# Optimization experiments

Measured on AMD Instinct MI355X. Metric: run time of the kernel, lower is better.

The kernel has to match this reference:

```python
import jax, jax.numpy as jnp
import numpy as np

DIM = 1024
H = 16
DH = DIM // H
NF = 64
EPS = 1e-6


def setup_inputs() -> dict:
    key = jax.random.key(0)
    ks = jax.random.split(key, 10)
    B, L = 4, 4096
    s = 1.0 / np.sqrt(DIM)
    x = jax.random.normal(ks[0], (B, L, DIM), dtype=jnp.float32)
    Wq = jax.random.normal(ks[1], (DIM, DIM), dtype=jnp.float32) * s
    Wk = jax.random.normal(ks[2], (DIM, DIM), dtype=jnp.float32) * s
    Wv = jax.random.normal(ks[3], (DIM, DIM), dtype=jnp.float32) * s
    Wo = jax.random.normal(ks[4], (DIM, DIM), dtype=jnp.float32) * s
    bq = jax.random.normal(ks[5], (DIM,), dtype=jnp.float32) * s
    bk = jax.random.normal(ks[6], (DIM,), dtype=jnp.float32) * s
    bv = jax.random.normal(ks[7], (DIM,), dtype=jnp.float32) * s
    bo = jax.random.normal(ks[8], (DIM,), dtype=jnp.float32) * s
    # random-feature buffer: [num_repeats=1, H, DH, NF]; use repeat 0
    Wrf = jax.random.normal(ks[9], (1, H, DH, NF), dtype=jnp.float32)
    return {"x": x, "Wq": Wq, "bq": bq, "Wk": Wk, "bk": bk, "Wv": Wv,
            "bv": bv, "Wo": Wo, "bo": bo, "Wrf": Wrf}


def reference(x, Wq, bq, Wk, bk, Wv, bv, Wo, bo, Wrf):
    B, L, _ = x.shape
    W0 = Wrf[0]  # [H, DH, NF]

    def split_heads(y):
        return y.reshape(B, L, H, DH).transpose(0, 2, 1, 3)  # [B,H,L,DH]

    q = split_heads(x @ Wq.T + bq)
    k = split_heads(x @ Wk.T + bk)
    v = split_heads(x @ Wv.T + bv)

    # key summary: logits [B,H,L,NF], softmax over flattened (L*NF)
    logits = jnp.einsum('bhld,hdf->bhlf', k, W0) \
             - 0.5 * jnp.sum(k * k, axis=-1, keepdims=True)
    alpha = jax.nn.softmax(logits.reshape(B, H, L * NF), axis=2)
    alpha = alpha.reshape(B, H, L, NF)
    N = jnp.einsum('bhlf,bhld->bhfd', alpha, v)  # [B,H,NF,DH]
    D = jnp.sum(alpha, axis=2)                   # [B,H,NF]

    # query feature map: per-position softmax over features
    phi = jax.nn.softmax(jnp.einsum('bhld,hdf->bhlf', q, W0), axis=-1)

    num = jnp.einsum('bhlf,bhfd->bhld', phi, N)
    den = jnp.einsum('bhlf,bhf->bhl', phi, D)
    out = num / (den[..., None] + EPS)

    ctx = out.transpose(0, 2, 1, 3).reshape(B, L, DIM)
    return ctx @ Wo.T + bo
```

## Files before the change

### kernel.cpp

```cpp
#include <hip/hip_runtime.h>
#include <hip/hip_bf16.h>

constexpr int NB   = 4;
constexpr int SL   = 4096;
constexpr int DIMC = 1024;
constexpr int NH   = 16;
constexpr int DHC  = 64;
constexpr int NFC  = 64;
constexpr int NCHK = 8;
constexpr float FEPS = 1e-6f;

typedef __attribute__((ext_vector_type(8))) short bf16x8_t;
typedef __attribute__((ext_vector_type(4))) float f32x4_t;
typedef __attribute__((ext_vector_type(4))) short s16x4_t;

__device__ __forceinline__ void load_lds_16B(const short* g, short* l) {
  __builtin_amdgcn_global_load_lds(
      (__attribute__((address_space(1))) void*)(g),
      (__attribute__((address_space(3))) void*)(l), 16, 0, 0);
}

__global__ __launch_bounds__(256) void cast_f32_to_bf16(
    const float* __restrict__ in, short* __restrict__ out, int n)
{
  const int i = (blockIdx.x * 256 + threadIdx.x) * 4;
  if (i >= n) return;
  const f32x4_t v = *(const f32x4_t*)(in + i);
  s16x4_t o;
#pragma unroll
  for (int j = 0; j < 4; j++) {
    __hip_bfloat16 h = __float2bfloat16(v[j]);
    o[j] = *(short*)&h;
  }
  *(s16x4_t*)(out + i) = o;
}

__global__ __launch_bounds__(256) void prep_w0t_kernel(
    const float* __restrict__ Wrf, short* __restrict__ Whi, short* __restrict__ Wlo)
{
  const int h = blockIdx.x;
  for (int t = threadIdx.x; t < 4096; t += 256) {
    const int f = t >> 6, dh = t & 63;
    const float w = Wrf[(size_t)h * 4096 + dh * 64 + f];
    __hip_bfloat16 hi = __float2bfloat16(w);
    const float rem = w - __bfloat162float(hi);
    __hip_bfloat16 lo = __float2bfloat16(rem);
    Whi[(size_t)h * 4096 + t] = *(short*)&hi;
    Wlo[(size_t)h * 4096 + t] = *(short*)&lo;
  }
}

__global__ __launch_bounds__(256) void fuse_w0_kernel(
    const float* __restrict__ Wq, const float* __restrict__ bq,
    const float* __restrict__ Wrf,
    short* __restrict__ Wfh, short* __restrict__ Wfl, float* __restrict__ bqf)
{
  const int h = blockIdx.x, cb = blockIdx.y;
  __shared__ float sWq[64][64];
  __shared__ float sW0[64][64];
  for (int idx = threadIdx.x; idx < 4096; idx += 256) {
    const int d = idx >> 6, e = idx & 63;
    sWq[d][e] = Wq[(size_t)(h * 64 + d) * 1024 + cb * 64 + e];
    sW0[d][e] = Wrf[(size_t)h * 4096 + d * 64 + e];
  }
  __syncthreads();
  for (int idx = threadIdx.x; idx < 4096; idx += 256) {
    const int f = idx >> 6, cc = idx & 63;
    float acc = 0.f;
#pragma unroll
    for (int d = 0; d < 64; d++) acc = fmaf(sWq[d][cc], sW0[d][f], acc);
    const __hip_bfloat16 hi = __float2bfloat16(acc);
    const float rem = acc - __bfloat162float(hi);
    const __hip_bfloat16 lo = __float2bfloat16(rem);
    Wfh[(size_t)(h * 64 + f) * 1024 + cb * 64 + cc] = *(const short*)&hi;
    Wfl[(size_t)(h * 64 + f) * 1024 + cb * 64 + cc] = *(const short*)&lo;
  }
  if (cb == 0 && threadIdx.x < 64) {
    const int f = threadIdx.x;
    float acc = 0.f;
#pragma unroll
    for (int d = 0; d < 64; d++) acc = fmaf(bq[h * 64 + d], sW0[d][f], acc);
    bqf[h * 64 + f] = acc;
  }
}

template <int MODE>
__global__ __launch_bounds__(256) void gemm_lds_kernel(
    const short* __restrict__ A, const short* __restrict__ W,
    const float* __restrict__ bias, void* __restrict__ C0,
    void* __restrict__ C1, float* __restrict__ Ks)
{
  constexpr int K = 1024, N = 1024;
  const int lane = threadIdx.x & 63;
  const int wid  = threadIdx.x >> 6;
  const int sub  = lane & 15;
  const int quad = lane >> 4;
  const int wr   = (wid >> 1) * 64;
  const int wc   = (wid & 1) * 64;
  const int row0 = blockIdx.x * 128;
  const int col0 = blockIdx.y * 128;

  __shared__ short As[128 * 64];
  __shared__ short Bs[128 * 64];

  f32x4_t acc[4][4] = {};

  const int srow = lane >> 3;
  for (int k0 = 0; k0 < K; k0 += 64) {
#pragma unroll
    for (int t = 0; t < 4; t++) {
      const int R   = wid * 32 + t * 8;
      const int row = R + srow;
      const int c   = (lane & 7) ^ (row & 7);
      load_lds_16B(A + (size_t)(row0 + row) * K + k0 + c * 8, As + R * 64);
      load_lds_16B(W + (size_t)(col0 + row) * K + k0 + c * 8, Bs + R * 64);
    }
    __syncthreads();

    bf16x8_t a[2][4], b[2][4];
#pragma unroll
    for (int ks = 0; ks < 2; ks++) {
#pragma unroll
      for (int i = 0; i < 4; i++) {
        const int ra = wr + i * 16 + sub;
        a[ks][i] = *(const bf16x8_t*)(As + ra * 64 + (((ks * 4 + quad) ^ (ra & 7)) * 8));
        const int rb = wc + i * 16 + sub;
        b[ks][i] = *(const bf16x8_t*)(Bs + rb * 64 + (((ks * 4 + quad) ^ (rb & 7)) * 8));
      }
    }
#pragma unroll
    for (int ks = 0; ks < 2; ks++)
#pragma unroll
      for (int i = 0; i < 4; i++)
#pragma unroll
        for (int j = 0; j < 4; j++) {
          if constexpr (MODE == 5)
            acc[i][j] = __builtin_amdgcn_mfma_f32_16x16x32_bf16(b[ks][j], a[ks][i], acc[i][j], 0, 0, 0);
          else
            acc[i][j] = __builtin_amdgcn_mfma_f32_16x16x32_bf16(a[ks][i], b[ks][j], acc[i][j], 0, 0, 0);
        }
    __syncthreads();
  }

  const int rb0 = row0 + wr;
  const int cb0 = col0 + wc;
  if constexpr (MODE == 3) {
    __hip_bfloat16* chi = (__hip_bfloat16*)C0;
    __hip_bfloat16* clo = (__hip_bfloat16*)C1;
    float s[4][4];
#pragma unroll
    for (int i = 0; i < 4; i++)
#pragma unroll
      for (int r = 0; r < 4; r++) s[i][r] = 0.f;
#pragma unroll
    for (int j = 0; j < 4; j++) {
      const int col = cb0 + j * 16 + sub;
      const float bv = bias[col];
#pragma unroll
      for (int i = 0; i < 4; i++) {
        const int row = rb0 + i * 16 + quad * 4;
#pragma unroll
        for (int r = 0; r < 4; r++) {
          const float val = acc[i][j][r] + bv;
          const __hip_bfloat16 hi = __float2bfloat16(val);
          const float rem = val - __bfloat162float(hi);
          chi[(size_t)(row + r) * N + col] = hi;
          clo[(size_t)(row + r) * N + col] = __float2bfloat16(rem);
          s[i][r] = fmaf(val, val, s[i][r]);
        }
      }
    }
    {
      const int head = cb0 >> 6;
#pragma unroll
      for (int o = 1; o < 16; o <<= 1)
#pragma unroll
        for (int i = 0; i < 4; i++)
#pragma unroll
          for (int r = 0; r < 4; r++) s[i][r] += __shfl_xor(s[i][r], o);
      if (sub == 0) {
#pragma unroll
        for (int i = 0; i < 4; i++)
#pragma unroll
          for (int r = 0; r < 4; r++)
            Ks[(size_t)(rb0 + i * 16 + quad * 4 + r) * NH + head] = s[i][r];
      }
    }
  } else if constexpr (MODE == 5) {
    __hip_bfloat16* vT = (__hip_bfloat16*)C0;
    const int bb    = row0 >> 12;
    const int lbase = rb0 - (bb << 12);
#pragma unroll
    for (int j = 0; j < 4; j++) {
#pragma unroll
      for (int r = 0; r < 4; r++) {
        const int col = cb0 + j * 16 + quad * 4 + r;
        const int h = col >> 6, d = col & 63;
        const float bv = bias[col];
        const size_t rowbase = ((size_t)((bb * NH + h) * 64 + d)) * (size_t)SL;
#pragma unroll
        for (int i = 0; i < 4; i++) {
          const int l = lbase + i * 16 + sub;
          const int pos = (l & ~127) | (((((l >> 3) & 15) ^ (d & 15)) << 3) | (l & 7));
          vT[rowbase + pos] = __float2bfloat16(acc[i][j][r] + bv);
        }
      }
    }
  } else {
#pragma unroll
    for (int j = 0; j < 4; j++) {
      const int col = cb0 + j * 16 + sub;
      const float bv = bias[col];
#pragma unroll
      for (int i = 0; i < 4; i++) {
        const int row = rb0 + i * 16 + quad * 4;
#pragma unroll
        for (int r = 0; r < 4; r++) {
          const float val = acc[i][j][r] + bv;
          ((float*)C0)[(size_t)(row + r) * N + col] = val;
        }
      }
    }
  }
}

__global__ __launch_bounds__(256) void gemm_phi_kernel(
    const short* __restrict__ A, const short* __restrict__ Wh,
    const short* __restrict__ Wl, const float* __restrict__ bqf,
    const float* __restrict__ Df, short* __restrict__ ehi,
    short* __restrict__ elo, float* __restrict__ sbuf)
{
  constexpr int K = 1024;
  const int lane = threadIdx.x & 63;
  const int wid  = threadIdx.x >> 6;
  const int sub  = lane & 15;
  const int quad = lane >> 4;
  const int wr   = (wid >> 1) * 64;
  const int wc   = (wid & 1) * 64;
  const int row0 = blockIdx.x * 128;
  const int col0 = blockIdx.y * 128;

  __shared__ short As[128 * 64];
  __shared__ short Bhs[128 * 64];
  __shared__ short Bls[128 * 64];

  f32x4_t acc[4][4] = {};

  const int srow = lane >> 3;
  for (int k0 = 0; k0 < K; k0 += 64) {
#pragma unroll
    for (int t = 0; t < 4; t++) {
      const int R   = wid * 32 + t * 8;
      const int row = R + srow;
      const int c   = (lane & 7) ^ (row & 7);
      load_lds_16B(A  + (size_t)(row0 + row) * K + k0 + c * 8, As  + R * 64);
      load_lds_16B(Wh + (size_t)(col0 + row) * K + k0 + c * 8, Bhs + R * 64);
      load_lds_16B(Wl + (size_t)(col0 + row) * K + k0 + c * 8, Bls + R * 64);
    }
    __syncthreads();

#pragma unroll
    for (int ks = 0; ks < 2; ks++) {
      bf16x8_t a[4], bh[4], bl[4];
#pragma unroll
      for (int i = 0; i < 4; i++) {
        const int ra = wr + i * 16 + sub;
        a[i] = *(const bf16x8_t*)(As + ra * 64 + (((ks * 4 + quad) ^ (ra & 7)) * 8));
        const int rb = wc + i * 16 + sub;
        bh[i] = *(const bf16x8_t*)(Bhs + rb * 64 + (((ks * 4 + quad) ^ (rb & 7)) * 8));
        bl[i] = *(const bf16x8_t*)(Bls + rb * 64 + (((ks * 4 + quad) ^ (rb & 7)) * 8));
      }
#pragma unroll
      for (int i = 0; i < 4; i++)
#pragma unroll
        for (int j = 0; j < 4; j++) {
          acc[i][j] = __builtin_amdgcn_mfma_f32_16x16x32_bf16(a[i], bh[j], acc[i][j], 0, 0, 0);
          acc[i][j] = __builtin_amdgcn_mfma_f32_16x16x32_bf16(a[i], bl[j], acc[i][j], 0, 0, 0);
        }
      __syncthreads();
    }
  }

  const int rb0 = row0 + wr;
  const int cb0 = col0 + wc;
  const int b   = row0 >> 12;
  const int h   = cb0 >> 6;
  float bv[4], Dl[4];
#pragma unroll
  for (int j = 0; j < 4; j++) {
    const int f = j * 16 + sub;
    bv[j] = bqf[h * 64 + f];
    Dl[j] = Df[(b * NH + h) * 64 + f];
  }
#pragma unroll
  for (int i = 0; i < 4; i++) {
#pragma unroll
    for (int r = 0; r < 4; r++) {
      float v[4];
#pragma unroll
      for (int j = 0; j < 4; j++) v[j] = acc[i][j][r] + bv[j];
      float mx = fmaxf(fmaxf(v[0], v[1]), fmaxf(v[2], v[3]));
#pragma unroll
      for (int o = 1; o < 16; o <<= 1) mx = fmaxf(mx, __shfl_xor(mx, o));
      float e[4], se = 0.f, dt = 0.f;
#pragma unroll
      for (int j = 0; j < 4; j++) {
        e[j] = __expf(v[j] - mx);
        se += e[j];
        dt = fmaf(e[j], Dl[j], dt);
      }
#pragma unroll
      for (int o = 1; o < 16; o <<= 1) { se += __shfl_xor(se, o); dt += __shfl_xor(dt, o); }

      const int row = rb0 + i * 16 + quad * 4 + r;
      const size_t base = (size_t)row * DIMC + h * 64;
#pragma unroll
      for (int j = 0; j < 4; j++) {
        const __hip_bfloat16 hi = __float2bfloat16(e[j]);
        const float rem = e[j] - __bfloat162float(hi);
        const __hip_bfloat16 lo = __float2bfloat16(rem);
        ehi[base + j * 16 + sub] = *(const short*)&hi;
        elo[base + j * 16 + sub] = *(const short*)&lo;
      }
      if (sub == 0) sbuf[row * NH + h] = 1.f / (dt + FEPS * se);
    }
  }
}

__global__ __launch_bounds__(256) void kv_fused_kernel(
    const short* __restrict__ khi, const short* __restrict__ klo,
    const short* __restrict__ W0h, const short* __restrict__ W0l,
    const float* __restrict__ ksq, const short* __restrict__ vT,
    float* __restrict__ pN, float* __restrict__ pD)
{
  const int chunk = blockIdx.x, h = blockIdx.y, b = blockIdx.z;
  const int tid  = threadIdx.x;
  const int lane = tid & 63, wid = tid >> 6;
  const int sub  = lane & 15, quad = lane >> 4;

  __shared__ short vTs[64 * 128];
  __shared__ short w0hs[64 * 64];
  __shared__ short w0ls[64 * 64];
  __shared__ short uh[128 * 64];
  __shared__ short ul[128 * 64];

  f32x4_t accN[4] = {};
  f32x4_t accD = {};
  bf16x8_t bones;
#pragma unroll
  for (int e = 0; e < 8; e++) bones[e] = (sub == 0) ? (short)0x3F80 : (short)0;

#pragma unroll
  for (int t = 0; t < 2; t++) {
    const int R   = wid * 16 + t * 8;
    const int row = R + (lane >> 3);
    const int c   = (lane & 7) ^ (row & 7);
    load_lds_16B(W0h + (size_t)h * 4096 + row * 64 + c * 8, w0hs + R * 64);
    load_lds_16B(W0l + (size_t)h * 4096 + row * 64 + c * 8, w0ls + R * 64);
  }

  const size_t vbase = ((size_t)((b * NH + h) * 64)) * (size_t)SL;
  const int fbase = (wid * 16 + sub) * 128;

  for (int it = 0; it < 4; ++it) {
    const int l0 = chunk * 512 + it * 128;

#pragma unroll
    for (int q = 0; q < 4; q++) {
      const int dbase = wid * 16 + q * 4;
      const int d = dbase + (lane >> 4);
      load_lds_16B(vT + vbase + (size_t)d * SL + l0 + (lane & 15) * 8,
                   vTs + dbase * 128);
    }
#pragma unroll
    for (int t = 0; t < 4; t++) {
      const int R   = wid * 32 + t * 8;
      const int row = R + (lane >> 3);
      const int c   = (lane & 7) ^ (row & 7);
      const size_t src = (size_t)(b * SL + l0 + row) * DIMC + h * 64 + c * 8;
      load_lds_16B(khi + src, uh + R * 64);
      load_lds_16B(klo + src, ul + R * 64);
    }
    __syncthreads();

    f32x4_t kacc[2][4] = {};
#pragma unroll
    for (int ks = 0; ks < 2; ks++) {
      bf16x8_t ah[2], al[2], b0[4], b1[4];
#pragma unroll
      for (int i = 0; i < 2; i++) {
        const int ra  = wid * 32 + i * 16 + sub;
        const int off = ra * 64 + (((ks * 4 + quad) ^ (ra & 7)) * 8);
        ah[i] = *(const bf16x8_t*)(uh + off);
        al[i] = *(const bf16x8_t*)(ul + off);
      }
#pragma unroll
      for (int j = 0; j < 4; j++) {
        const int rb  = j * 16 + sub;
        const int off = rb * 64 + (((ks * 4 + quad) ^ (rb & 7)) * 8);
        b0[j] = *(const bf16x8_t*)(w0hs + off);
        b1[j] = *(const bf16x8_t*)(w0ls + off);
      }
#pragma unroll
      for (int i = 0; i < 2; i++)
#pragma unroll
        for (int j = 0; j < 4; j++) {
          kacc[i][j] = __builtin_amdgcn_mfma_f32_16x16x32_bf16(ah[i], b0[j], kacc[i][j], 0, 0, 0);
          kacc[i][j] = __builtin_amdgcn_mfma_f32_16x16x32_bf16(al[i], b0[j], kacc[i][j], 0, 0, 0);
          kacc[i][j] = __builtin_amdgcn_mfma_f32_16x16x32_bf16(ah[i], b1[j], kacc[i][j], 0, 0, 0);
        }
    }
    __syncthreads();

#pragma unroll
    for (int i = 0; i < 2; i++) {
#pragma unroll
      for (int r = 0; r < 4; r++) {
        const int tok = wid * 32 + i * 16 + quad * 4 + r;
        const float kq = 0.5f * ksq[(size_t)(b * SL + l0 + tok) * NH + h];
#pragma unroll
        for (int j = 0; j < 4; j++) {
          const int f = j * 16 + sub;
          const float wv = __expf(kacc[i][j][r] - kq);
          const __hip_bfloat16 hi = __float2bfloat16(wv);
          const float rem = wv - __bfloat162float(hi);
          const __hip_bfloat16 lo = __float2bfloat16(rem);
          const int p = f * 128 + (((((tok >> 3) & 15) ^ (f & 15)) << 3) | (tok & 7));
          uh[p] = *(const short*)&hi;
          ul[p] = *(const short*)&lo;
        }
      }
    }
    __syncthreads();

#pragma unroll
    for (int ks = 0; ks < 4; ks++) {
      const int ch = ks * 4 + quad;
      const bf16x8_t ah = *(const bf16x8_t*)(uh + fbase + ((ch ^ sub) << 3));
      const bf16x8_t al = *(const bf16x8_t*)(ul + fbase + ((ch ^ sub) << 3));
      accD = __builtin_amdgcn_mfma_f32_16x16x32_bf16(ah, bones, accD, 0, 0, 0);
      accD = __builtin_amdgcn_mfma_f32_16x16x32_bf16(al, bones, accD, 0, 0, 0);
#pragma unroll
      for (int j = 0; j < 4; j++) {
        const bf16x8_t bv = *(const bf16x8_t*)(vTs + (j * 16 + sub) * 128 + ((ch ^ sub) << 3));
        accN[j] = __builtin_amdgcn_mfma_f32_16x16x32_bf16(ah, bv, accN[j], 0, 0, 0);
        accN[j] = __builtin_amdgcn_mfma_f32_16x16x32_bf16(al, bv, accN[j], 0, 0, 0);
      }
    }
    __syncthreads();
  }

  const size_t pbase = (size_t)((b * NH + h) * NCHK + chunk);
#pragma unroll
  for (int j = 0; j < 4; j++)
#pragma unroll
    for (int r = 0; r < 4; r++)
      pN[pbase * 4096 + (wid * 16 + quad * 4 + r) * 64 + j * 16 + sub] = accN[j][r];
  if (sub == 0) {
#pragma unroll
    for (int r = 0; r < 4; r++)
      pD[pbase * 64 + wid * 16 + quad * 4 + r] = accD[r];
  }
}

__global__ __launch_bounds__(256) void combine_nd_kernel(
    const float* __restrict__ pN, const float* __restrict__ pD,
    short* __restrict__ NfTh, short* __restrict__ NfTl, float* __restrict__ Df)
{
  const int bh = blockIdx.x, seg = blockIdx.y;
  __shared__ float sInv;
  float dsum = 0.f;
  if (threadIdx.x < 64) {
    for (int c = 0; c < NCHK; c++)
      dsum += pD[(size_t)(bh * NCHK + c) * 64 + threadIdx.x];
    float s = dsum;
#pragma unroll
    for (int o = 32; o; o >>= 1) s += __shfl_xor(s, o);
    if (threadIdx.x == 0) sInv = 1.f / s;
  }
  __syncthreads();
  const float inv = sInv;
  if (seg == 0 && threadIdx.x < 64) Df[bh * 64 + threadIdx.x] = dsum * inv;
  const int t = seg * 256 + threadIdx.x;
  float acc = 0.f;
  for (int c = 0; c < NCHK; c++)
    acc += pN[((size_t)(bh * NCHK + c)) * 4096 + t];
  const float val = acc * inv;
  const int f = t >> 6, d = t & 63;
  const __hip_bfloat16 hi = __float2bfloat16(val);
  const float rem = val - __bfloat162float(hi);
  const __hip_bfloat16 lo = __float2bfloat16(rem);
  NfTh[(size_t)bh * 4096 + d * 64 + f] = *(const short*)&hi;
  NfTl[(size_t)bh * 4096 + d * 64 + f] = *(const short*)&lo;
}

__global__ __launch_bounds__(256) void ctx_gemm_kernel(
    const short* __restrict__ ehi, const short* __restrict__ elo,
    const short* __restrict__ NfTh, const short* __restrict__ NfTl,
    const float* __restrict__ sbuf, __hip_bfloat16* __restrict__ ctx)
{
  const int lane = threadIdx.x & 63, wid = threadIdx.x >> 6;
  const int sub = lane & 15, quad = lane >> 4;
  const int h = blockIdx.y;
  const int tok0 = blockIdx.x * 128 + wid * 32;
  const int b = blockIdx.x >> 5;
  const short* Bh = NfTh + ((size_t)(b * NH + h)) * 4096;
  const short* Bl = NfTl + ((size_t)(b * NH + h)) * 4096;

  f32x4_t acc[2][4] = {};
#pragma unroll
  for (int ks = 0; ks < 2; ks++) {
    const int ko = ks * 32 + quad * 8;
    bf16x8_t ah[2], al[2], bh[4], bl[4];
#pragma unroll
    for (int i = 0; i < 2; i++) {
      const size_t base = (size_t)(tok0 + i * 16 + sub) * DIMC + h * 64 + ko;
      ah[i] = *(const bf16x8_t*)(ehi + base);
      al[i] = *(const bf16x8_t*)(elo + base);
    }
#pragma unroll
    for (int j = 0; j < 4; j++) {
      const size_t base = (size_t)(j * 16 + sub) * 64 + ko;
      bh[j] = *(const bf16x8_t*)(Bh + base);
      bl[j] = *(const bf16x8_t*)(Bl + base);
    }
#pragma unroll
    for (int i = 0; i < 2; i++)
#pragma unroll
      for (int j = 0; j < 4; j++) {
        acc[i][j] = __builtin_amdgcn_mfma_f32_16x16x32_bf16(ah[i], bh[j], acc[i][j], 0, 0, 0);
        acc[i][j] = __builtin_amdgcn_mfma_f32_16x16x32_bf16(al[i], bh[j], acc[i][j], 0, 0, 0);
        acc[i][j] = __builtin_amdgcn_mfma_f32_16x16x32_bf16(ah[i], bl[j], acc[i][j], 0, 0, 0);
      }
  }
#pragma unroll
  for (int i = 0; i < 2; i++)
#pragma unroll
    for (int r = 0; r < 4; r++) {
      const int token = tok0 + i * 16 + quad * 4 + r;
      const float sv = sbuf[token * NH + h];
#pragma unroll
      for (int j = 0; j < 4; j++)
        ctx[(size_t)token * DIMC + h * 64 + j * 16 + sub] =
            __float2bfloat16(acc[i][j][r] * sv);
    }
}

extern "C" void kernel_launch(void* const* d_in, const int* in_sizes, int n_in,
                              void* d_out, int out_size, void* d_ws, size_t ws_size,
                              hipStream_t stream) {
  (void)in_sizes; (void)n_in; (void)out_size; (void)ws_size;
  const float* x   = (const float*)d_in[0];
  const float* Wq  = (const float*)d_in[1];
  const float* bq  = (const float*)d_in[2];
  const float* Wk  = (const float*)d_in[3];
  const float* bk  = (const float*)d_in[4];
  const float* Wv  = (const float*)d_in[5];
  const float* bv  = (const float*)d_in[6];
  const float* Wo  = (const float*)d_in[7];
  const float* bo  = (const float*)d_in[8];
  const float* Wrf = (const float*)d_in[9];
  float* out = (float*)d_out;

  constexpr size_t MiB = 1u << 20;
  constexpr size_t KiB = 1u << 10;
  constexpr size_t NTOK = (size_t)NB * SL;
  constexpr size_t XN   = NTOK * DIMC;
  constexpr size_t WN   = (size_t)DIMC * DIMC;

  char* ws = (char*)d_ws;
  short* xb   = (short*)(ws);
  short* Wkb  = (short*)(ws + 32 * MiB);
  short* Wvb  = (short*)(ws + 34 * MiB);
  short* Wob  = (short*)(ws + 36 * MiB);
  short* W0Th = (short*)(ws + 40 * MiB);
  short* W0Tl = (short*)(ws + 40 * MiB + 128 * KiB);
  float* bqf  = (float*)(ws + 40 * MiB + 256 * KiB);
  float* ksq  = (float*)(ws + 41 * MiB);
  float* sbuf = (float*)(ws + 42 * MiB);
  float* pD   = (float*)(ws + 43 * MiB);
  short* NfTh = (short*)(ws + 43 * MiB + 512 * KiB);
  short* NfTl = (short*)(ws + 44 * MiB);
  float* Df   = (float*)(ws + 44 * MiB + 512 * KiB);
  float* pN   = (float*)(ws + 45 * MiB);
  __hip_bfloat16* khi = (__hip_bfloat16*)(ws + 109 * MiB);
  __hip_bfloat16* klo = (__hip_bfloat16*)(ws + 141 * MiB);
  short* vTb  = (short*)(ws + 173 * MiB);
  short* Wqfh = (short*)(ws + 173 * MiB);
  short* Wqfl = (short*)(ws + 175 * MiB);
  short* ehi  = (short*)(ws + 45 * MiB);
  short* elo  = (short*)(ws + 77 * MiB);
  __hip_bfloat16* ctxb = (__hip_bfloat16*)xb;

  const dim3 blk(256);

  cast_f32_to_bf16<<<dim3(XN / 1024), blk, 0, stream>>>(x, xb, (int)XN);
  cast_f32_to_bf16<<<dim3(WN / 1024), blk, 0, stream>>>(Wk, Wkb, (int)WN);
  cast_f32_to_bf16<<<dim3(WN / 1024), blk, 0, stream>>>(Wv, Wvb, (int)WN);
  cast_f32_to_bf16<<<dim3(WN / 1024), blk, 0, stream>>>(Wo, Wob, (int)WN);
  prep_w0t_kernel<<<dim3(NH), blk, 0, stream>>>(Wrf, W0Th, W0Tl);

  const dim3 gg(NTOK / 128, DIMC / 128);
  gemm_lds_kernel<3><<<gg, blk, 0, stream>>>(xb, Wkb, bk, khi, klo, ksq);
  gemm_lds_kernel<5><<<gg, blk, 0, stream>>>(xb, Wvb, bv, vTb, nullptr, nullptr);

  kv_fused_kernel<<<dim3(NCHK, NH, NB), blk, 0, stream>>>(
      (const short*)khi, (const short*)klo, W0Th, W0Tl, ksq, vTb, pN, pD);
  fuse_w0_kernel<<<dim3(NH, 16), blk, 0, stream>>>(Wq, bq, Wrf, Wqfh, Wqfl, bqf);
  combine_nd_kernel<<<dim3(NB * NH, 16), blk, 0, stream>>>(pN, pD, NfTh, NfTl, Df);

  gemm_phi_kernel<<<gg, blk, 0, stream>>>(xb, Wqfh, Wqfl, bqf, Df, ehi, elo, sbuf);
  ctx_gemm_kernel<<<dim3(NTOK / 128, NH), blk, 0, stream>>>(
      ehi, elo, NfTh, NfTl, sbuf, ctxb);

  gemm_lds_kernel<0><<<gg, blk, 0, stream>>>((const short*)ctxb, Wob, bo, out, nullptr, nullptr);
}
```

Measured before the change: 459.5 us.

## Fuse K and V projection GEMMs into one kernel sharing A tiles; merge weight casts

```diff
diff --git a/kernel.cpp b/kernel.cpp
--- a/kernel.cpp
+++ b/kernel.cpp
@@ -25,6 +25,24 @@
 {
   const int i = (blockIdx.x * 256 + threadIdx.x) * 4;
   if (i >= n) return;
+  const f32x4_t v = *(const f32x4_t*)(in + i);
+  s16x4_t o;
+#pragma unroll
+  for (int j = 0; j < 4; j++) {
+    __hip_bfloat16 h = __float2bfloat16(v[j]);
+    o[j] = *(short*)&h;
+  }
+  *(s16x4_t*)(out + i) = o;
+}
+
+__global__ __launch_bounds__(256) void cast3_kernel(
+    const float* __restrict__ a, const float* __restrict__ b,
+    const float* __restrict__ c, short* __restrict__ oa,
+    short* __restrict__ ob, short* __restrict__ oc)
+{
+  const float* in  = blockIdx.y == 0 ? a : (blockIdx.y == 1 ? b : c);
+  short*       out = blockIdx.y == 0 ? oa : (blockIdx.y == 1 ? ob : oc);
+  const int i = (blockIdx.x * 256 + threadIdx.x) * 4;
   const f32x4_t v = *(const f32x4_t*)(in + i);
   s16x4_t o;
 #pragma unroll
@@ -84,11 +102,9 @@
   }
 }
 
-template <int MODE>
-__global__ __launch_bounds__(256) void gemm_lds_kernel(
+__global__ __launch_bounds__(256) void gemm_out_kernel(
     const short* __restrict__ A, const short* __restrict__ W,
-    const float* __restrict__ bias, void* __restrict__ C0,
-    void* __restrict__ C1, float* __restrict__ Ks)
+    const float* __restrict__ bias, float* __restrict__ C0)
 {
   constexpr int K = 1024, N = 1024;
   const int lane = threadIdx.x & 63;
@@ -133,20 +149,100 @@
 #pragma unroll
       for (int i = 0; i < 4; i++)
 #pragma unroll
-        for (int j = 0; j < 4; j++) {
-          if constexpr (MODE == 5)
-            acc[i][j] = __builtin_amdgcn_mfma_f32_16x16x32_bf16(b[ks][j], a[ks][i], acc[i][j], 0, 0, 0);
-          else
-            acc[i][j] = __builtin_amdgcn_mfma_f32_16x16x32_bf16(a[ks][i], b[ks][j], acc[i][j], 0, 0, 0);
-        }
+        for (int j = 0; j < 4; j++)
+          acc[i][j] = __builtin_amdgcn_mfma_f32_16x16x32_bf16(a[ks][i], b[ks][j], acc[i][j], 0, 0, 0);
     __syncthreads();
   }
 
   const int rb0 = row0 + wr;
   const int cb0 = col0 + wc;
-  if constexpr (MODE == 3) {
-    __hip_bfloat16* chi = (__hip_bfloat16*)C0;
-    __hip_bfloat16* clo = (__hip_bfloat16*)C1;
+#pragma unroll
+  for (int j = 0; j < 4; j++) {
+    const int col = cb0 + j * 16 + sub;
+    const float bv = bias[col];
+#pragma unroll
+    for (int i = 0; i < 4; i++) {
+      const int row = rb0 + i * 16 + quad * 4;
+#pragma unroll
+      for (int r = 0; r < 4; r++)
+        C0[(size_t)(row + r) * N + col] = acc[i][j][r] + bv;
+    }
+  }
+}
+
+__global__ __launch_bounds__(256) void gemm_kv_kernel(
+    const short* __restrict__ A, const short* __restrict__ Wk,
+    const short* __restrict__ Wv, const float* __restrict__ bk,
+    const float* __restrict__ bv,
+    __hip_bfloat16* __restrict__ chi, __hip_bfloat16* __restrict__ clo,
+    float* __restrict__ Ks, __hip_bfloat16* __restrict__ vT)
+{
+  constexpr int K = 1024, N = 1024;
+  const int lane = threadIdx.x & 63;
+  const int wid  = threadIdx.x >> 6;
+  const int sub  = lane & 15;
+  const int quad = lane >> 4;
+  const int wr   = (wid >> 1) * 64;
+  const int wc   = (wid & 1) * 64;
+  const int row0 = blockIdx.x * 128;
+  const int col0 = blockIdx.y * 128;
+
+  __shared__ short As[128 * 64];
+  __shared__ short Bks[128 * 64];
+  __shared__ short Bvs[128 * 64];
+
+  f32x4_t accK[4][4] = {};
+  f32x4_t accV[4][4] = {};
+
+  const int srow = lane >> 3;
+  for (int k0 = 0; k0 < K; k0 += 64) {
+#pragma unroll
+    for (int t = 0; t < 4; t++) {
+      const int R   = wid * 32 + t * 8;
+      const int row = R + srow;
+      const int c   = (lane & 7) ^ (row & 7);
+      load_lds_16B(A  + (size_t)(row0 + row) * K + k0 + c * 8, As  + R * 64);
+      load_lds_16B(Wk + (size_t)(col0 + row) * K + k0 + c * 8, Bks + R * 64);
+      load_lds_16B(Wv + (size_t)(col0 + row) * K + k0 + c * 8, Bvs + R * 64);
+    }
+    __syncthreads();
+
+#pragma unroll
+    for (int ks = 0; ks < 2; ks++) {
+      bf16x8_t a[4], bb[4];
+#pragma unroll
+      for (int i = 0; i < 4; i++) {
+        const int ra = wr + i * 16 + sub;
+        a[i] = *(const bf16x8_t*)(As + ra * 64 + (((ks * 4 + quad) ^ (ra & 7)) * 8));
+      }
+#pragma unroll
+      for (int j = 0; j < 4; j++) {
+        const int rb = wc + j * 16 + sub;
+        bb[j] = *(const bf16x8_t*)(Bks + rb * 64 + (((ks * 4 + quad) ^ (rb & 7)) * 8));
+      }
+#pragma unroll
+      for (int i = 0; i < 4; i++)
+#pragma unroll
+        for (int j = 0; j < 4; j++)
+          accK[i][j] = __builtin_amdgcn_mfma_f32_16x16x32_bf16(a[i], bb[j], accK[i][j], 0, 0, 0);
+#pragma unroll
+      for (int j = 0; j < 4; j++) {
+        const int rb = wc + j * 16 + sub;
+        bb[j] = *(const bf16x8_t*)(Bvs + rb * 64 + (((ks * 4 + quad) ^ (rb & 7)) * 8));
+      }
+#pragma unroll
+      for (int i = 0; i < 4; i++)
+#pragma unroll
+        for (int j = 0; j < 4; j++)
+          accV[i][j] = __builtin_amdgcn_mfma_f32_16x16x32_bf16(bb[j], a[i], accV[i][j], 0, 0, 0);
+    }
+    __syncthreads();
+  }
+
+  const int rb0 = row0 + wr;
+  const int cb0 = col0 + wc;
+
+  {
     float s[4][4];
 #pragma unroll
     for (int i = 0; i < 4; i++)
@@ -155,13 +251,13 @@
 #pragma unroll
     for (int j = 0; j < 4; j++) {
       const int col = cb0 + j * 16 + sub;
-      const float bv = bias[col];
+      const float bvv = bk[col];
 #pragma unroll
       for (int i = 0; i < 4; i++) {
         const int row = rb0 + i * 16 + quad * 4;
 #pragma unroll
         for (int r = 0; r < 4; r++) {
-          const float val = acc[i][j][r] + bv;
+          const float val = accK[i][j][r] + bvv;
           const __hip_bfloat16 hi = __float2bfloat16(val);
           const float rem = val - __bfloat162float(hi);
           chi[(size_t)(row + r) * N + col] = hi;
@@ -170,24 +266,23 @@
         }
       }
     }
-    {
-      const int head = cb0 >> 6;
-#pragma unroll
-      for (int o = 1; o < 16; o <<= 1)
-#pragma unroll
-        for (int i = 0; i < 4; i++)
-#pragma unroll
-          for (int r = 0; r < 4; r++) s[i][r] += __shfl_xor(s[i][r], o);
-      if (sub == 0) {
-#pragma unroll
-        for (int i = 0; i < 4; i++)
-#pragma unroll
-          for (int r = 0; r < 4; r++)
-            Ks[(size_t)(rb0 + i * 16 + quad * 4 + r) * NH + head] = s[i][r];
-      }
-    }
-  } else if constexpr (MODE == 5) {
-    __hip_bfloat16* vT = (__hip_bfloat16*)C0;
+    const int head = cb0 >> 6;
+#pragma unroll
+    for (int o = 1; o < 16; o <<= 1)
+#pragma unroll
+      for (int i = 0; i < 4; i++)
+#pragma unroll
+        for (int r = 0; r < 4; r++) s[i][r] += __shfl_xor(s[i][r], o);
+    if (sub == 0) {
+#pragma unroll
+      for (int i = 0; i < 4; i++)
+#pragma unroll
+        for (int r = 0; r < 4; r++)
+          Ks[(size_t)(rb0 + i * 16 + quad * 4 + r) * NH + head] = s[i][r];
+    }
+  }
+
+  {
     const int bb    = row0 >> 12;
     const int lbase = rb0 - (bb << 12);
 #pragma unroll
@@ -196,28 +291,13 @@
       for (int r = 0; r < 4; r++) {
         const int col = cb0 + j * 16 + quad * 4 + r;
         const int h = col >> 6, d = col & 63;
-        const float bv = bias[col];
+        const float bvv = bv[col];
         const size_t rowbase = ((size_t)((bb * NH + h) * 64 + d)) * (size_t)SL;
 #pragma unroll
         for (int i = 0; i < 4; i++) {
           const int l = lbase + i * 16 + sub;
           const int pos = (l & ~127) | (((((l >> 3) & 15) ^ (d & 15)) << 3) | (l & 7));
-          vT[rowbase + pos] = __float2bfloat16(acc[i][j][r] + bv);
-        }
-      }
-    }
-  } else {
-#pragma unroll
-    for (int j = 0; j < 4; j++) {
-      const int col = cb0 + j * 16 + sub;
-      const float bv = bias[col];
-#pragma unroll
-      for (int i = 0; i < 4; i++) {
-        const int row = rb0 + i * 16 + quad * 4;
-#pragma unroll
-        for (int r = 0; r < 4; r++) {
-          const float val = acc[i][j][r] + bv;
-          ((float*)C0)[(size_t)(row + r) * N + col] = val;
+          vT[rowbase + pos] = __float2bfloat16(accV[i][j][r] + bvv);
         }
       }
     }
@@ -595,14 +675,12 @@
   const dim3 blk(256);
 
   cast_f32_to_bf16<<<dim3(XN / 1024), blk, 0, stream>>>(x, xb, (int)XN);
-  cast_f32_to_bf16<<<dim3(WN / 1024), blk, 0, stream>>>(Wk, Wkb, (int)WN);
-  cast_f32_to_bf16<<<dim3(WN / 1024), blk, 0, stream>>>(Wv, Wvb, (int)WN);
-  cast_f32_to_bf16<<<dim3(WN / 1024), blk, 0, stream>>>(Wo, Wob, (int)WN);
+  cast3_kernel<<<dim3(WN / 1024, 3), blk, 0, stream>>>(Wk, Wv, Wo, Wkb, Wvb, Wob);
   prep_w0t_kernel<<<dim3(NH), blk, 0, stream>>>(Wrf, W0Th, W0Tl);
 
   const dim3 gg(NTOK / 128, DIMC / 128);
-  gemm_lds_kernel<3><<<gg, blk, 0, stream>>>(xb, Wkb, bk, khi, klo, ksq);
-  gemm_lds_kernel<5><<<gg, blk, 0, stream>>>(xb, Wvb, bv, vTb, nullptr, nullptr);
+  gemm_kv_kernel<<<gg, blk, 0, stream>>>(xb, Wkb, Wvb, bk, bv,
+                                         khi, klo, ksq, (__hip_bfloat16*)vTb);
 
   kv_fused_kernel<<<dim3(NCHK, NH, NB), blk, 0, stream>>>(
       (const short*)khi, (const short*)klo, W0Th, W0Tl, ksq, vTb, pN, pD);
@@ -613,5 +691,5 @@
   ctx_gemm_kernel<<<dim3(NTOK / 128, NH), blk, 0, stream>>>(
       ehi, elo, NfTh, NfTl, sbuf, ctxb);
 
-  gemm_lds_kernel<0><<<gg, blk, 0, stream>>>((const short*)ctxb, Wob, bo, out, nullptr, nullptr);
-}
+  gemm_out_kernel<<<gg, blk, 0, stream>>>((const short*)ctxb, Wob, bo, out);
+}
```

Result: slower. 468.7 us (+2.0%).

## Use double-buffered 256x256 GEMM tiles and merge weight casts into one launch

Applied to the files above, without the earlier changes.

```diff
diff --git a/kernel.cpp b/kernel.cpp
--- a/kernel.cpp
+++ b/kernel.cpp
@@ -25,6 +25,24 @@
 {
   const int i = (blockIdx.x * 256 + threadIdx.x) * 4;
   if (i >= n) return;
+  const f32x4_t v = *(const f32x4_t*)(in + i);
+  s16x4_t o;
+#pragma unroll
+  for (int j = 0; j < 4; j++) {
+    __hip_bfloat16 h = __float2bfloat16(v[j]);
+    o[j] = *(short*)&h;
+  }
+  *(s16x4_t*)(out + i) = o;
+}
+
+__global__ __launch_bounds__(256) void cast3_kernel(
+    const float* __restrict__ a, const float* __restrict__ b,
+    const float* __restrict__ c, short* __restrict__ oa,
+    short* __restrict__ ob, short* __restrict__ oc)
+{
+  const float* in  = blockIdx.y == 0 ? a : (blockIdx.y == 1 ? b : c);
+  short*       out = blockIdx.y == 0 ? oa : (blockIdx.y == 1 ? ob : oc);
+  const int i = (blockIdx.x * 256 + threadIdx.x) * 4;
   const f32x4_t v = *(const f32x4_t*)(in + i);
   s16x4_t o;
 #pragma unroll
@@ -85,7 +103,7 @@
 }
 
 template <int MODE>
-__global__ __launch_bounds__(256) void gemm_lds_kernel(
+__global__ __launch_bounds__(512) void gemm256_kernel(
     const short* __restrict__ A, const short* __restrict__ W,
     const float* __restrict__ bias, void* __restrict__ C0,
     void* __restrict__ C1, float* __restrict__ Ks)
@@ -95,61 +113,84 @@
   const int wid  = threadIdx.x >> 6;
   const int sub  = lane & 15;
   const int quad = lane >> 4;
-  const int wr   = (wid >> 1) * 64;
-  const int wc   = (wid & 1) * 64;
-  const int row0 = blockIdx.x * 128;
-  const int col0 = blockIdx.y * 128;
-
-  __shared__ short As[128 * 64];
-  __shared__ short Bs[128 * 64];
-
-  f32x4_t acc[4][4] = {};
+  const int wm   = wid >> 2;
+  const int wn   = wid & 3;
+  const int row0 = blockIdx.x * 256;
+  const int col0 = blockIdx.y * 256;
+
+  __shared__ short As[2][256 * 64];
+  __shared__ short Bs[2][256 * 64];
+
+  f32x4_t acc[8][4] = {};
 
   const int srow = lane >> 3;
-  for (int k0 = 0; k0 < K; k0 += 64) {
+
+  auto STAGE = [&](int bu, int kt) {
+    const int k0 = kt * 64;
 #pragma unroll
     for (int t = 0; t < 4; t++) {
       const int R   = wid * 32 + t * 8;
       const int row = R + srow;
       const int c   = (lane & 7) ^ (row & 7);
-      load_lds_16B(A + (size_t)(row0 + row) * K + k0 + c * 8, As + R * 64);
-      load_lds_16B(W + (size_t)(col0 + row) * K + k0 + c * 8, Bs + R * 64);
-    }
-    __syncthreads();
-
-    bf16x8_t a[2][4], b[2][4];
+      load_lds_16B(A + (size_t)(row0 + row) * K + k0 + c * 8, &As[bu][R * 64]);
+      load_lds_16B(W + (size_t)(col0 + row) * K + k0 + c * 8, &Bs[bu][R * 64]);
+    }
+  };
+
+  STAGE(0, 0);
+  asm volatile("s_waitcnt vmcnt(0)" ::: "memory");
+  __builtin_amdgcn_s_barrier();
+  asm volatile("" ::: "memory");
+
+  for (int kt = 0; kt < 16; ++kt) {
+    const int cur = kt & 1;
+    if (kt < 15) {
+      STAGE(cur ^ 1, kt + 1);
+      asm volatile("s_waitcnt vmcnt(8)" ::: "memory");
+    } else {
+      asm volatile("s_waitcnt vmcnt(0)" ::: "memory");
+    }
+    __builtin_amdgcn_s_barrier();
+    asm volatile("" ::: "memory");
+
 #pragma unroll
     for (int ks = 0; ks < 2; ks++) {
-#pragma unroll
-      for (int i = 0; i < 4; i++) {
-        const int ra = wr + i * 16 + sub;
-        a[ks][i] = *(const bf16x8_t*)(As + ra * 64 + (((ks * 4 + quad) ^ (ra & 7)) * 8));
-        const int rb = wc + i * 16 + sub;
-        b[ks][i] = *(const bf16x8_t*)(Bs + rb * 64 + (((ks * 4 + quad) ^ (rb & 7)) * 8));
-      }
-    }
-#pragma unroll
-    for (int ks = 0; ks < 2; ks++)
-#pragma unroll
-      for (int i = 0; i < 4; i++)
+      bf16x8_t a[8], b[4];
+#pragma unroll
+      for (int i = 0; i < 8; i++) {
+        const int ra = wm * 128 + i * 16 + sub;
+        a[i] = *(const bf16x8_t*)(&As[cur][ra * 64 + (((ks * 4 + quad) ^ (ra & 7)) * 8)]);
+      }
+#pragma unroll
+      for (int j = 0; j < 4; j++) {
+        const int rb = wn * 64 + j * 16 + sub;
+        b[j] = *(const bf16x8_t*)(&Bs[cur][rb * 64 + (((ks * 4 + quad) ^ (rb & 7)) * 8)]);
+      }
+      __builtin_amdgcn_s_setprio(1);
+#pragma unroll
+      for (int i = 0; i < 8; i++)
 #pragma unroll
         for (int j = 0; j < 4; j++) {
           if constexpr (MODE == 5)
-            acc[i][j] = __builtin_amdgcn_mfma_f32_16x16x32_bf16(b[ks][j], a[ks][i], acc[i][j], 0, 0, 0);
+            acc[i][j] = __builtin_amdgcn_mfma_f32_16x16x32_bf16(b[j], a[i], acc[i][j], 0, 0, 0);
           else
-            acc[i][j] = __builtin_amdgcn_mfma_f32_16x16x32_bf16(a[ks][i], b[ks][j], acc[i][j], 0, 0, 0);
+            acc[i][j] = __builtin_amdgcn_mfma_f32_16x16x32_bf16(a[i], b[j], acc[i][j], 0, 0, 0);
         }
-    __syncthreads();
-  }
-
-  const int rb0 = row0 + wr;
-  const int cb0 = col0 + wc;
+      __builtin_amdgcn_s_setprio(0);
+    }
+    asm volatile("s_waitcnt lgkmcnt(0)" ::: "memory");
+    __builtin_amdgcn_s_barrier();
+    asm volatile("" ::: "memory");
+  }
+
+  const int rb0 = row0 + wm * 128;
+  const int cb0 = col0 + wn * 64;
   if constexpr (MODE == 3) {
     __hip_bfloat16* chi = (__hip_bfloat16*)C0;
     __hip_bfloat16* clo = (__hip_bfloat16*)C1;
-    float s[4][4];
-#pragma unroll
-    for (int i = 0; i < 4; i++)
+    float s[8][4];
+#pragma unroll
+    for (int i = 0; i < 8; i++)
 #pragma unroll
       for (int r = 0; r < 4; r++) s[i][r] = 0.f;
 #pragma unroll
@@ -157,7 +198,7 @@
       const int col = cb0 + j * 16 + sub;
       const float bv = bias[col];
 #pragma unroll
-      for (int i = 0; i < 4; i++) {
+      for (int i = 0; i < 8; i++) {
         const int row = rb0 + i * 16 + quad * 4;
 #pragma unroll
         for (int r = 0; r < 4; r++) {
@@ -170,21 +211,19 @@
         }
       }
     }
-    {
-      const int head = cb0 >> 6;
-#pragma unroll
-      for (int o = 1; o < 16; o <<= 1)
-#pragma unroll
-        for (int i = 0; i < 4; i++)
-#pragma unroll
-          for (int r = 0; r < 4; r++) s[i][r] += __shfl_xor(s[i][r], o);
-      if (sub == 0) {
-#pragma unroll
-        for (int i = 0; i < 4; i++)
-#pragma unroll
-          for (int r = 0; r < 4; r++)
-            Ks[(size_t)(rb0 + i * 16 + quad * 4 + r) * NH + head] = s[i][r];
-      }
+    const int head = cb0 >> 6;
+#pragma unroll
+    for (int o = 1; o < 16; o <<= 1)
+#pragma unroll
+      for (int i = 0; i < 8; i++)
+#pragma unroll
+        for (int r = 0; r < 4; r++) s[i][r] += __shfl_xor(s[i][r], o);
+    if (sub == 0) {
+#pragma unroll
+      for (int i = 0; i < 8; i++)
+#pragma unroll
+        for (int r = 0; r < 4; r++)
+          Ks[(size_t)(rb0 + i * 16 + quad * 4 + r) * NH + head] = s[i][r];
     }
   } else if constexpr (MODE == 5) {
     __hip_bfloat16* vT = (__hip_bfloat16*)C0;
@@ -199,7 +238,7 @@
         const float bv = bias[col];
         const size_t rowbase = ((size_t)((bb * NH + h) * 64 + d)) * (size_t)SL;
 #pragma unroll
-        for (int i = 0; i < 4; i++) {
+        for (int i = 0; i < 8; i++) {
           const int l = lbase + i * 16 + sub;
           const int pos = (l & ~127) | (((((l >> 3) & 15) ^ (d & 15)) << 3) | (l & 7));
           vT[rowbase + pos] = __float2bfloat16(acc[i][j][r] + bv);
@@ -212,13 +251,11 @@
       const int col = cb0 + j * 16 + sub;
       const float bv = bias[col];
 #pragma unroll
-      for (int i = 0; i < 4; i++) {
+      for (int i = 0; i < 8; i++) {
         const int row = rb0 + i * 16 + quad * 4;
 #pragma unroll
-        for (int r = 0; r < 4; r++) {
-          const float val = acc[i][j][r] + bv;
-          ((float*)C0)[(size_t)(row + r) * N + col] = val;
-        }
+        for (int r = 0; r < 4; r++)
+          ((float*)C0)[(size_t)(row + r) * N + col] = acc[i][j][r] + bv;
       }
     }
   }
@@ -593,25 +630,25 @@
   __hip_bfloat16* ctxb = (__hip_bfloat16*)xb;
 
   const dim3 blk(256);
+  const dim3 blk512(512);
 
   cast_f32_to_bf16<<<dim3(XN / 1024), blk, 0, stream>>>(x, xb, (int)XN);
-  cast_f32_to_bf16<<<dim3(WN / 1024), blk, 0, stream>>>(Wk, Wkb, (int)WN);
-  cast_f32_to_bf16<<<dim3(WN / 1024), blk, 0, stream>>>(Wv, Wvb, (int)WN);
-  cast_f32_to_bf16<<<dim3(WN / 1024), blk, 0, stream>>>(Wo, Wob, (int)WN);
+  cast3_kernel<<<dim3(WN / 1024, 3), blk, 0, stream>>>(Wk, Wv, Wo, Wkb, Wvb, Wob);
   prep_w0t_kernel<<<dim3(NH), blk, 0, stream>>>(Wrf, W0Th, W0Tl);
 
-  const dim3 gg(NTOK / 128, DIMC / 128);
-  gemm_lds_kernel<3><<<gg, blk, 0, stream>>>(xb, Wkb, bk, khi, klo, ksq);
-  gemm_lds_kernel<5><<<gg, blk, 0, stream>>>(xb, Wvb, bv, vTb, nullptr, nullptr);
+  const dim3 g256(NTOK / 256, DIMC / 256);
+  gemm256_kernel<3><<<g256, blk512, 0, stream>>>(xb, Wkb, bk, khi, klo, ksq);
+  gemm256_kernel<5><<<g256, blk512, 0, stream>>>(xb, Wvb, bv, vTb, nullptr, nullptr);
 
   kv_fused_kernel<<<dim3(NCHK, NH, NB), blk, 0, stream>>>(
       (const short*)khi, (const short*)klo, W0Th, W0Tl, ksq, vTb, pN, pD);
   fuse_w0_kernel<<<dim3(NH, 16), blk, 0, stream>>>(Wq, bq, Wrf, Wqfh, Wqfl, bqf);
   combine_nd_kernel<<<dim3(NB * NH, 16), blk, 0, stream>>>(pN, pD, NfTh, NfTl, Df);
 
+  const dim3 gg(NTOK / 128, DIMC / 128);
   gemm_phi_kernel<<<gg, blk, 0, stream>>>(xb, Wqfh, Wqfl, bqf, Df, ehi, elo, sbuf);
   ctx_gemm_kernel<<<dim3(NTOK / 128, NH), blk, 0, stream>>>(
       ehi, elo, NfTh, NfTl, sbuf, ctxb);
 
-  gemm_lds_kernel<0><<<gg, blk, 0, stream>>>((const short*)ctxb, Wob, bo, out, nullptr, nullptr);
-}
+  gemm256_kernel<0><<<g256, blk512, 0, stream>>>((const short*)ctxb, Wob, bo, out, nullptr, nullptr);
+}
```

Result: slower. 476.6 us (+3.7%).

## Fuse query feature softmax with context GEMM through LDS, batch weight casts

Applied to the files above, without the earlier changes.

```diff
diff --git a/kernel.cpp b/kernel.cpp
--- a/kernel.cpp
+++ b/kernel.cpp
@@ -25,6 +25,24 @@
 {
   const int i = (blockIdx.x * 256 + threadIdx.x) * 4;
   if (i >= n) return;
+  const f32x4_t v = *(const f32x4_t*)(in + i);
+  s16x4_t o;
+#pragma unroll
+  for (int j = 0; j < 4; j++) {
+    __hip_bfloat16 h = __float2bfloat16(v[j]);
+    o[j] = *(short*)&h;
+  }
+  *(s16x4_t*)(out + i) = o;
+}
+
+__global__ __launch_bounds__(256) void cast3_kernel(
+    const float* __restrict__ a, const float* __restrict__ b,
+    const float* __restrict__ c, short* __restrict__ oa,
+    short* __restrict__ ob, short* __restrict__ oc)
+{
+  const float* in  = blockIdx.y == 0 ? a : (blockIdx.y == 1 ? b : c);
+  short*       out = blockIdx.y == 0 ? oa : (blockIdx.y == 1 ? ob : oc);
+  const int i = (blockIdx.x * 256 + threadIdx.x) * 4;
   const f32x4_t v = *(const f32x4_t*)(in + i);
   s16x4_t o;
 #pragma unroll
@@ -224,11 +242,11 @@
   }
 }
 
-__global__ __launch_bounds__(256) void gemm_phi_kernel(
+__global__ __launch_bounds__(256, 3) void gemm_phi_ctx_kernel(
     const short* __restrict__ A, const short* __restrict__ Wh,
     const short* __restrict__ Wl, const float* __restrict__ bqf,
-    const float* __restrict__ Df, short* __restrict__ ehi,
-    short* __restrict__ elo, float* __restrict__ sbuf)
+    const float* __restrict__ Df, const short* __restrict__ NfTh,
+    const short* __restrict__ NfTl, __hip_bfloat16* __restrict__ ctx)
 {
   constexpr int K = 1024;
   const int lane = threadIdx.x & 63;
@@ -285,45 +303,96 @@
   const int cb0 = col0 + wc;
   const int b   = row0 >> 12;
   const int h   = cb0 >> 6;
-  float bv[4], Dl[4];
+  float bvv[4], Dl[4];
 #pragma unroll
   for (int j = 0; j < 4; j++) {
     const int f = j * 16 + sub;
-    bv[j] = bqf[h * 64 + f];
-    Dl[j] = Df[(b * NH + h) * 64 + f];
-  }
-#pragma unroll
-  for (int i = 0; i < 4; i++) {
-#pragma unroll
-    for (int r = 0; r < 4; r++) {
-      float v[4];
-#pragma unroll
-      for (int j = 0; j < 4; j++) v[j] = acc[i][j][r] + bv[j];
-      float mx = fmaxf(fmaxf(v[0], v[1]), fmaxf(v[2], v[3]));
-#pragma unroll
-      for (int o = 1; o < 16; o <<= 1) mx = fmaxf(mx, __shfl_xor(mx, o));
-      float e[4], se = 0.f, dt = 0.f;
+    bvv[j] = bqf[h * 64 + f];
+    Dl[j]  = Df[(b * NH + h) * 64 + f];
+  }
+
+  short* ewh = Bhs + wid * 2048;
+  short* ewl = Bls + wid * 2048;
+  const short* Nh = NfTh + ((size_t)(b * NH + h)) * 4096;
+  const short* Nl = NfTl + ((size_t)(b * NH + h)) * 4096;
+
+  for (int half = 0; half < 2; ++half) {
+    __syncthreads();
+    float svh[2][4];
+#pragma unroll
+    for (int i2 = 0; i2 < 2; i2++) {
+      const int i = half * 2 + i2;
+#pragma unroll
+      for (int r = 0; r < 4; r++) {
+        float v[4];
+#pragma unroll
+        for (int j = 0; j < 4; j++) v[j] = acc[i][j][r] + bvv[j];
+        float mx = fmaxf(fmaxf(v[0], v[1]), fmaxf(v[2], v[3]));
+#pragma unroll
+        for (int o = 1; o < 16; o <<= 1) mx = fmaxf(mx, __shfl_xor(mx, o));
+        float e[4], se = 0.f, dt = 0.f;
+#pragma unroll
+        for (int j = 0; j < 4; j++) {
+          e[j] = __expf(v[j] - mx);
+          se += e[j];
+          dt = fmaf(e[j], Dl[j], dt);
+        }
+#pragma unroll
+        for (int o = 1; o < 16; o <<= 1) { se += __shfl_xor(se, o); dt += __shfl_xor(dt, o); }
+        svh[i2][r] = 1.f / (dt + FEPS * se);
+
+        const int lrow = i2 * 16 + quad * 4 + r;
+#pragma unroll
+        for (int j = 0; j < 4; j++) {
+          const int f = j * 16 + sub;
+          const __hip_bfloat16 hi = __float2bfloat16(e[j]);
+          const float rem = e[j] - __bfloat162float(hi);
+          const __hip_bfloat16 lo = __float2bfloat16(rem);
+          const int p = lrow * 64 + ((((f >> 3) ^ (lrow & 7)) << 3) | (f & 7));
+          ewh[p] = *(const short*)&hi;
+          ewl[p] = *(const short*)&lo;
+        }
+      }
+    }
+    __syncthreads();
+
+    f32x4_t cacc[2][4] = {};
+#pragma unroll
+    for (int ks = 0; ks < 2; ks++) {
+      bf16x8_t ah[2], al[2], nh[4], nl[4];
+#pragma unroll
+      for (int i2 = 0; i2 < 2; i2++) {
+        const int lrow = i2 * 16 + sub;
+        const int off = lrow * 64 + (((ks * 4 + quad) ^ (lrow & 7)) << 3);
+        ah[i2] = *(const bf16x8_t*)(ewh + off);
+        al[i2] = *(const bf16x8_t*)(ewl + off);
+      }
 #pragma unroll
       for (int j = 0; j < 4; j++) {
-        e[j] = __expf(v[j] - mx);
-        se += e[j];
-        dt = fmaf(e[j], Dl[j], dt);
-      }
-#pragma unroll
-      for (int o = 1; o < 16; o <<= 1) { se += __shfl_xor(se, o); dt += __shfl_xor(dt, o); }
-
-      const int row = rb0 + i * 16 + quad * 4 + r;
-      const size_t base = (size_t)row * DIMC + h * 64;
-#pragma unroll
-      for (int j = 0; j < 4; j++) {
-        const __hip_bfloat16 hi = __float2bfloat16(e[j]);
-        const float rem = e[j] - __bfloat162float(hi);
-        const __hip_bfloat16 lo = __float2bfloat16(rem);
-        ehi[base + j * 16 + sub] = *(const short*)&hi;
-        elo[base + j * 16 + sub] = *(const short*)&lo;
-      }
-      if (sub == 0) sbuf[row * NH + h] = 1.f / (dt + FEPS * se);
-    }
+        const size_t nb = (size_t)(j * 16 + sub) * 64 + ks * 32 + quad * 8;
+        nh[j] = *(const bf16x8_t*)(Nh + nb);
+        nl[j] = *(const bf16x8_t*)(Nl + nb);
+      }
+#pragma unroll
+      for (int i2 = 0; i2 < 2; i2++)
+#pragma unroll
+        for (int j = 0; j < 4; j++) {
+          cacc[i2][j] = __builtin_amdgcn_mfma_f32_16x16x32_bf16(ah[i2], nh[j], cacc[i2][j], 0, 0, 0);
+          cacc[i2][j] = __builtin_amdgcn_mfma_f32_16x16x32_bf16(al[i2], nh[j], cacc[i2][j], 0, 0, 0);
+          cacc[i2][j] = __builtin_amdgcn_mfma_f32_16x16x32_bf16(ah[i2], nl[j], cacc[i2][j], 0, 0, 0);
+        }
+    }
+#pragma unroll
+    for (int i2 = 0; i2 < 2; i2++)
+#pragma unroll
+      for (int r = 0; r < 4; r++) {
+        const int token = rb0 + half * 32 + i2 * 16 + quad * 4 + r;
+        const float sv = svh[i2][r];
+#pragma unroll
+        for (int j = 0; j < 4; j++)
+          ctx[(size_t)token * DIMC + h * 64 + j * 16 + sub] =
+              __float2bfloat16(cacc[i2][j][r] * sv);
+      }
   }
 }
 
@@ -492,58 +561,6 @@
   const __hip_bfloat16 lo = __float2bfloat16(rem);
   NfTh[(size_t)bh * 4096 + d * 64 + f] = *(const short*)&hi;
   NfTl[(size_t)bh * 4096 + d * 64 + f] = *(const short*)&lo;
-}
-
-__global__ __launch_bounds__(256) void ctx_gemm_kernel(
-    const short* __restrict__ ehi, const short* __restrict__ elo,
-    const short* __restrict__ NfTh, const short* __restrict__ NfTl,
-    const float* __restrict__ sbuf, __hip_bfloat16* __restrict__ ctx)
-{
-  const int lane = threadIdx.x & 63, wid = threadIdx.x >> 6;
-  const int sub = lane & 15, quad = lane >> 4;
-  const int h = blockIdx.y;
-  const int tok0 = blockIdx.x * 128 + wid * 32;
-  const int b = blockIdx.x >> 5;
-  const short* Bh = NfTh + ((size_t)(b * NH + h)) * 4096;
-  const short* Bl = NfTl + ((size_t)(b * NH + h)) * 4096;
-
-  f32x4_t acc[2][4] = {};
-#pragma unroll
-  for (int ks = 0; ks < 2; ks++) {
-    const int ko = ks * 32 + quad * 8;
-    bf16x8_t ah[2], al[2], bh[4], bl[4];
-#pragma unroll
-    for (int i = 0; i < 2; i++) {
-      const size_t base = (size_t)(tok0 + i * 16 + sub) * DIMC + h * 64 + ko;
-      ah[i] = *(const bf16x8_t*)(ehi + base);
-      al[i] = *(const bf16x8_t*)(elo + base);
-    }
-#pragma unroll
-    for (int j = 0; j < 4; j++) {
-      const size_t base = (size_t)(j * 16 + sub) * 64 + ko;
-      bh[j] = *(const bf16x8_t*)(Bh + base);
-      bl[j] = *(const bf16x8_t*)(Bl + base);
-    }
-#pragma unroll
-    for (int i = 0; i < 2; i++)
-#pragma unroll
-      for (int j = 0; j < 4; j++) {
-        acc[i][j] = __builtin_amdgcn_mfma_f32_16x16x32_bf16(ah[i], bh[j], acc[i][j], 0, 0, 0);
-        acc[i][j] = __builtin_amdgcn_mfma_f32_16x16x32_bf16(al[i], bh[j], acc[i][j], 0, 0, 0);
-        acc[i][j] = __builtin_amdgcn_mfma_f32_16x16x32_bf16(ah[i], bl[j], acc[i][j], 0, 0, 0);
-      }
-  }
-#pragma unroll
-  for (int i = 0; i < 2; i++)
-#pragma unroll
-    for (int r = 0; r < 4; r++) {
-      const int token = tok0 + i * 16 + quad * 4 + r;
-      const float sv = sbuf[token * NH + h];
-#pragma unroll
-      for (int j = 0; j < 4; j++)
-        ctx[(size_t)token * DIMC + h * 64 + j * 16 + sub] =
-            __float2bfloat16(acc[i][j][r] * sv);
-    }
 }
 
 extern "C" void kernel_launch(void* const* d_in, const int* in_sizes, int n_in,
@@ -577,7 +594,6 @@
   short* W0Tl = (short*)(ws + 40 * MiB + 128 * KiB);
   float* bqf  = (float*)(ws + 40 * MiB + 256 * KiB);
   float* ksq  = (float*)(ws + 41 * MiB);
-  float* sbuf = (float*)(ws + 42 * MiB);
   float* pD   = (float*)(ws + 43 * MiB);
   short* NfTh = (short*)(ws + 43 * MiB + 512 * KiB);
   short* NfTl = (short*)(ws + 44 * MiB);
@@ -588,16 +604,12 @@
   short* vTb  = (short*)(ws + 173 * MiB);
   short* Wqfh = (short*)(ws + 173 * MiB);
   short* Wqfl = (short*)(ws + 175 * MiB);
-  short* ehi  = (short*)(ws + 45 * MiB);
-  short* elo  = (short*)(ws + 77 * MiB);
-  __hip_bfloat16* ctxb = (__hip_bfloat16*)xb;
+  __hip_bfloat16* ctxb = (__hip_bfloat16*)khi;
 
   const dim3 blk(256);
 
   cast_f32_to_bf16<<<dim3(XN / 1024), blk, 0, stream>>>(x, xb, (int)XN);
-  cast_f32_to_bf16<<<dim3(WN / 1024), blk, 0, stream>>>(Wk, Wkb, (int)WN);
-  cast_f32_to_bf16<<<dim3(WN / 1024), blk, 0, stream>>>(Wv, Wvb, (int)WN);
-  cast_f32_to_bf16<<<dim3(WN / 1024), blk, 0, stream>>>(Wo, Wob, (int)WN);
+  cast3_kernel<<<dim3(WN / 1024, 3), blk, 0, stream>>>(Wk, Wv, Wo, Wkb, Wvb, Wob);
   prep_w0t_kernel<<<dim3(NH), blk, 0, stream>>>(Wrf, W0Th, W0Tl);
 
   const dim3 gg(NTOK / 128, DIMC / 128);
@@ -609,9 +621,8 @@
   fuse_w0_kernel<<<dim3(NH, 16), blk, 0, stream>>>(Wq, bq, Wrf, Wqfh, Wqfl, bqf);
   combine_nd_kernel<<<dim3(NB * NH, 16), blk, 0, stream>>>(pN, pD, NfTh, NfTl, Df);
 
-  gemm_phi_kernel<<<gg, blk, 0, stream>>>(xb, Wqfh, Wqfl, bqf, Df, ehi, elo, sbuf);
-  ctx_gemm_kernel<<<dim3(NTOK / 128, NH), blk, 0, stream>>>(
-      ehi, elo, NfTh, NfTl, sbuf, ctxb);
+  gemm_phi_ctx_kernel<<<gg, blk, 0, stream>>>(
+      xb, Wqfh, Wqfl, bqf, Df, NfTh, NfTl, ctxb);
 
   gemm_lds_kernel<0><<<gg, blk, 0, stream>>>((const short*)ctxb, Wob, bo, out, nullptr, nullptr);
 }
```

Result: slower. 479.7 us (+4.4%).
